# Kernel optimization log

Measured on AMD Instinct MI355X. Metric: run time of the kernel, lower is better.

Reference implementation:

```python
import jax, jax.numpy as jnp
import numpy as np

B, S, H = 32, 4096, 512

def setup_inputs() -> dict:
    key = jax.random.key(0)
    k1, k2, k3 = jax.random.split(key, 3)
    h_t = jax.random.normal(k1, (B, H), dtype=jnp.float32)
    context = jax.random.normal(k2, (B, S, H), dtype=jnp.float32)
    W = jax.random.normal(k3, (H, H), dtype=jnp.float32) * (1.0 / np.sqrt(H))
    pos = 7  # current cyclic-buffer write index (self.it % seq_len)
    return {"h_t": h_t, "context": context, "W": W, "pos": pos}

def reference(h_t, context, W, pos):
    # Luong 'general' attention: score[b,s] = h_t[b] . (W @ context[b,s])
    scores = jnp.einsum('bh,hk,bsk->bs', h_t, W, context)  # [B,S]
    attn = jax.nn.softmax(scores, axis=-1)                  # softmax over buffer slots
    # weighted sum over the context buffer -> [B,H]
    cntx = jnp.einsum('bs,bsh->bh', attn, context)
    # cyclic buffer write: add_vector(h_t) at slot pos (detached in original)
    new_buffer = context.at[:, pos % context.shape[1], :].set(h_t)
    return cntx, new_buffer
```

## Files before the change

### kernel.cpp

```cpp
#include <hip/hip_runtime.h>
#include <math.h>

constexpr int B = 32, S = 4096, H = 512;
constexpr int BDIM = 256;
constexpr int MAX_SPLIT = 128;
constexpr float LOG2E = 1.44269504088896340736f;
constexpr float DEFER_THR = 11.5415603f;

typedef float f4 __attribute__((ext_vector_type(4)));

__global__ __launch_bounds__(BDIM) void u_kernel(const float* __restrict__ h_t,
                                                 const float* __restrict__ W,
                                                 float* __restrict__ u) {
    const int b = blockIdx.y;
    const int k = blockIdx.x * BDIM + threadIdx.x;
    __shared__ float hs[H];
    for (int i = threadIdx.x; i < H; i += BDIM) hs[i] = h_t[b * H + i];
    __syncthreads();
    float a0 = 0.f, a1 = 0.f, a2 = 0.f, a3 = 0.f;
#pragma unroll 8
    for (int h = 0; h < H; h += 4) {
        a0 = fmaf(hs[h],     W[(size_t)(h)     * H + k], a0);
        a1 = fmaf(hs[h + 1], W[(size_t)(h + 1) * H + k], a1);
        a2 = fmaf(hs[h + 2], W[(size_t)(h + 2) * H + k], a2);
        a3 = fmaf(hs[h + 3], W[(size_t)(h + 3) * H + k], a3);
    }
    u[b * H + k] = ((a0 + a1) + (a2 + a3)) * LOG2E;
}

__global__ __launch_bounds__(BDIM) void flash_kernel(const float* __restrict__ ctx,
                                                     const float* __restrict__ u,
                                                     float* __restrict__ newbuf,
                                                     float* __restrict__ pacc,
                                                     float* __restrict__ pml,
                                                     int nsplit) {
    const int b     = blockIdx.y;
    const int split = blockIdx.x;
    const int w     = threadIdx.x >> 6;
    const int lane  = threadIdx.x & 63;
    const int g     = lane >> 5;
    const int j     = lane & 31;
    const int rpb   = S / nsplit;
    const int rpw   = rpb / 4;
    const int s0    = split * rpb + w * rpw;

    const f4* ub = (const f4*)(u + (size_t)b * H);
    f4 uf[4];
#pragma unroll
    for (int k = 0; k < 4; ++k) uf[k] = ub[j + 32 * k];

    float m = -INFINITY, l = 0.f;
    f4 acc[4] = {{0,0,0,0},{0,0,0,0},{0,0,0,0},{0,0,0,0}};

#pragma unroll 2
    for (int r = 0; r < rpw; r += 2) {
        const size_t row = (size_t)b * S + s0 + r + g;
        const f4* crow = (const f4*)(ctx + row * H);
        f4 c[4];
#pragma unroll
        for (int k = 0; k < 4; ++k) c[k] = crow[j + 32 * k];

        f4* orow = (f4*)(newbuf + row * H);
#pragma unroll
        for (int k = 0; k < 4; ++k)
            __builtin_nontemporal_store(c[k], orow + j + 32 * k);

        float d = c[0].x * uf[0].x;
        d = fmaf(c[0].y, uf[0].y, d); d = fmaf(c[0].z, uf[0].z, d);
        d = fmaf(c[0].w, uf[0].w, d);
#pragma unroll
        for (int k = 1; k < 4; ++k) {
            d = fmaf(c[k].x, uf[k].x, d); d = fmaf(c[k].y, uf[k].y, d);
            d = fmaf(c[k].z, uf[k].z, d); d = fmaf(c[k].w, uf[k].w, d);
        }
#pragma unroll
        for (int off = 16; off >= 1; off >>= 1) d += __shfl_xor(d, off);

        if (d > m + DEFER_THR) {
            const float sc = exp2f(m - d);
#pragma unroll
            for (int k = 0; k < 4; ++k) acc[k] *= sc;
            l *= sc; m = d;
        }
        const float p = exp2f(d - m);
#pragma unroll
        for (int k = 0; k < 4; ++k) acc[k] += p * c[k];
        l += p;
    }

    const float mo = __shfl_xor(m, 32);
    const float lo = __shfl_xor(l, 32);
    const float M  = fmaxf(m, mo);
    const float es = exp2f(m - M), eo = exp2f(mo - M);
    const float lw = es * l + eo * lo;
    f4 am[4];
#pragma unroll
    for (int k = 0; k < 4; ++k) {
        f4 other;
        other.x = __shfl_xor(acc[k].x, 32);
        other.y = __shfl_xor(acc[k].y, 32);
        other.z = __shfl_xor(acc[k].z, 32);
        other.w = __shfl_xor(acc[k].w, 32);
        am[k] = es * acc[k] + eo * other;
    }

    __shared__ float lacc[4][H];
    __shared__ float lml[4][2];
    if (g == 0) {
        f4* dst = (f4*)&lacc[w][0];
#pragma unroll
        for (int k = 0; k < 4; ++k) dst[j + 32 * k] = am[k];
        if (j == 0) { lml[w][0] = M; lml[w][1] = lw; }
    }
    __syncthreads();

    const float m0 = lml[0][0], m1 = lml[1][0], m2 = lml[2][0], m3 = lml[3][0];
    const float Mb = fmaxf(fmaxf(m0, m1), fmaxf(m2, m3));
    const float e0 = exp2f(m0 - Mb), e1 = exp2f(m1 - Mb);
    const float e2 = exp2f(m2 - Mb), e3 = exp2f(m3 - Mb);

    const int t    = threadIdx.x;
    const int pidx = b * nsplit + split;
    const float ca = e0 * lacc[0][t]       + e1 * lacc[1][t]
                   + e2 * lacc[2][t]       + e3 * lacc[3][t];
    const float cb = e0 * lacc[0][256 + t] + e1 * lacc[1][256 + t]
                   + e2 * lacc[2][256 + t] + e3 * lacc[3][256 + t];
    pacc[(size_t)pidx * H + t]       = ca;
    pacc[(size_t)pidx * H + 256 + t] = cb;
    if (t == 0) {
        const float L = e0 * lml[0][1] + e1 * lml[1][1]
                      + e2 * lml[2][1] + e3 * lml[3][1];
        pml[2 * pidx] = Mb; pml[2 * pidx + 1] = L;
    }
}

__global__ __launch_bounds__(BDIM) void combine_kernel(const float* __restrict__ pacc,
                                                       const float* __restrict__ pml,
                                                       const float* __restrict__ h_t,
                                                       const int* __restrict__ posp,
                                                       float* __restrict__ newbuf,
                                                       float* __restrict__ cntx,
                                                       int nsplit) {
    const int b    = blockIdx.x;
    const int half = blockIdx.y;
    const int t    = threadIdx.x;
    const int col  = half * 256 + t;

    int pos = posp[0] % S; if (pos < 0) pos += S;
    newbuf[((size_t)b * S + pos) * H + col] = h_t[b * H + col];

    __shared__ float lm[MAX_SPLIT], ll[MAX_SPLIT];
    for (int p = t; p < nsplit; p += BDIM) {
        lm[p] = pml[2 * (b * nsplit + p)];
        ll[p] = pml[2 * (b * nsplit + p) + 1];
    }
    __syncthreads();

    float M = -INFINITY;
    for (int p = 0; p < nsplit; ++p) M = fmaxf(M, lm[p]);

    float acc = 0.f, L = 0.f;
#pragma unroll 4
    for (int p = 0; p < nsplit; ++p) {
        const float e = exp2f(lm[p] - M);
        L   = fmaf(e, ll[p], L);
        acc = fmaf(e, pacc[(size_t)(b * nsplit + p) * H + col], acc);
    }
    cntx[b * H + col] = acc / L;
}

extern "C" void kernel_launch(void* const* d_in, const int* in_sizes, int n_in,
                              void* d_out, int out_size, void* d_ws, size_t ws_size,
                              hipStream_t stream) {
    const float* h_t = (const float*)d_in[0];
    const float* ctx = (const float*)d_in[1];
    const float* W   = (const float*)d_in[2];
    const int*   pos = (const int*)d_in[3];

    float* out    = (float*)d_out;
    float* cntx   = out;
    float* newbuf = out + (size_t)B * H;

    char*  ws = (char*)d_ws;
    float* u  = (float*)ws;
    const size_t u_bytes = (size_t)B * H * sizeof(float);

    int nsplit = MAX_SPLIT;
    while (nsplit > 1) {
        const size_t need = u_bytes
                          + (size_t)B * nsplit * H * sizeof(float)
                          + (size_t)B * nsplit * 2 * sizeof(float);
        if (need <= ws_size) break;
        nsplit >>= 1;
    }
    float* pacc = (float*)(ws + u_bytes);
    float* pml  = pacc + (size_t)B * nsplit * H;

    u_kernel<<<dim3(H / BDIM, B), BDIM, 0, stream>>>(h_t, W, u);
    flash_kernel<<<dim3(nsplit, B), BDIM, 0, stream>>>(ctx, u, newbuf,
                                                       pacc, pml, nsplit);
    combine_kernel<<<dim3(B, 2), BDIM, 0, stream>>>(pacc, pml, h_t, pos,
                                                    newbuf, cntx, nsplit);
}
```

Measured before the change: 122.2 us.

## Halve flash block size and interleave two independent online-softmax streams per wave

The flash kernel now runs 128 threads (2 waves) per block instead of 256. Each wave covers twice as many rows, split into two independent halves (A and B) with separate running max, sum and accumulator. Interleaving the two streams raises memory-level parallelism and ILP per wave, and the loop is fully unrolled. The cost is higher register pressure and fewer waves resident per block, with the per-block reduction rewritten for two waves and a vectorized partial write.

```diff
diff --git a/kernel.cpp b/kernel.cpp
--- a/kernel.cpp
+++ b/kernel.cpp
@@ -2,20 +2,21 @@
 #include <math.h>
 
 constexpr int B = 32, S = 4096, H = 512;
-constexpr int BDIM = 256;
+constexpr int UDIM = 256;
+constexpr int FDIM = 128;
 constexpr int MAX_SPLIT = 128;
 constexpr float LOG2E = 1.44269504088896340736f;
 constexpr float DEFER_THR = 11.5415603f;
 
 typedef float f4 __attribute__((ext_vector_type(4)));
 
-__global__ __launch_bounds__(BDIM) void u_kernel(const float* __restrict__ h_t,
+__global__ __launch_bounds__(UDIM) void u_kernel(const float* __restrict__ h_t,
                                                  const float* __restrict__ W,
                                                  float* __restrict__ u) {
     const int b = blockIdx.y;
-    const int k = blockIdx.x * BDIM + threadIdx.x;
+    const int k = blockIdx.x * UDIM + threadIdx.x;
     __shared__ float hs[H];
-    for (int i = threadIdx.x; i < H; i += BDIM) hs[i] = h_t[b * H + i];
+    for (int i = threadIdx.x; i < H; i += UDIM) hs[i] = h_t[b * H + i];
     __syncthreads();
     float a0 = 0.f, a1 = 0.f, a2 = 0.f, a3 = 0.f;
 #pragma unroll 8
@@ -28,7 +29,7 @@
     u[b * H + k] = ((a0 + a1) + (a2 + a3)) * LOG2E;
 }
 
-__global__ __launch_bounds__(BDIM) void flash_kernel(const float* __restrict__ ctx,
+__global__ __launch_bounds__(FDIM) void flash_kernel(const float* __restrict__ ctx,
                                                      const float* __restrict__ u,
                                                      float* __restrict__ newbuf,
                                                      float* __restrict__ pacc,
@@ -41,7 +42,8 @@
     const int g     = lane >> 5;
     const int j     = lane & 31;
     const int rpb   = S / nsplit;
-    const int rpw   = rpb / 4;
+    const int rpw   = rpb / 2;
+    const int hrw   = rpw / 2;
     const int s0    = split * rpb + w * rpw;
 
     const f4* ub = (const f4*)(u + (size_t)b * H);
@@ -49,98 +51,130 @@
 #pragma unroll
     for (int k = 0; k < 4; ++k) uf[k] = ub[j + 32 * k];
 
-    float m = -INFINITY, l = 0.f;
-    f4 acc[4] = {{0,0,0,0},{0,0,0,0},{0,0,0,0},{0,0,0,0}};
-
-#pragma unroll 2
-    for (int r = 0; r < rpw; r += 2) {
-        const size_t row = (size_t)b * S + s0 + r + g;
-        const f4* crow = (const f4*)(ctx + row * H);
-        f4 c[4];
-#pragma unroll
-        for (int k = 0; k < 4; ++k) c[k] = crow[j + 32 * k];
-
-        f4* orow = (f4*)(newbuf + row * H);
-#pragma unroll
-        for (int k = 0; k < 4; ++k)
-            __builtin_nontemporal_store(c[k], orow + j + 32 * k);
-
-        float d = c[0].x * uf[0].x;
-        d = fmaf(c[0].y, uf[0].y, d); d = fmaf(c[0].z, uf[0].z, d);
-        d = fmaf(c[0].w, uf[0].w, d);
+    const size_t baseA = (size_t)b * S + s0;
+    const size_t baseB = baseA + hrw;
+
+    float mA = -INFINITY, lA = 0.f;
+    float mB = -INFINITY, lB = 0.f;
+    f4 accA[4] = {{0,0,0,0},{0,0,0,0},{0,0,0,0},{0,0,0,0}};
+    f4 accB[4] = {{0,0,0,0},{0,0,0,0},{0,0,0,0},{0,0,0,0}};
+
+#pragma unroll
+    for (int r = 0; r < hrw; r += 2) {
+        const size_t rowA = baseA + r + g;
+        const size_t rowB = baseB + r + g;
+        const f4* cra = (const f4*)(ctx + rowA * H);
+        const f4* crb = (const f4*)(ctx + rowB * H);
+        f4 cA[4], cB[4];
+#pragma unroll
+        for (int k = 0; k < 4; ++k) cA[k] = cra[j + 32 * k];
+#pragma unroll
+        for (int k = 0; k < 4; ++k) cB[k] = crb[j + 32 * k];
+
+        f4* oa = (f4*)(newbuf + rowA * H);
+        f4* ob = (f4*)(newbuf + rowB * H);
+#pragma unroll
+        for (int k = 0; k < 4; ++k) {
+            __builtin_nontemporal_store(cA[k], oa + j + 32 * k);
+            __builtin_nontemporal_store(cB[k], ob + j + 32 * k);
+        }
+
+        float dA = cA[0].x * uf[0].x, dB = cB[0].x * uf[0].x;
+        dA = fmaf(cA[0].y, uf[0].y, dA); dB = fmaf(cB[0].y, uf[0].y, dB);
+        dA = fmaf(cA[0].z, uf[0].z, dA); dB = fmaf(cB[0].z, uf[0].z, dB);
+        dA = fmaf(cA[0].w, uf[0].w, dA); dB = fmaf(cB[0].w, uf[0].w, dB);
 #pragma unroll
         for (int k = 1; k < 4; ++k) {
-            d = fmaf(c[k].x, uf[k].x, d); d = fmaf(c[k].y, uf[k].y, d);
-            d = fmaf(c[k].z, uf[k].z, d); d = fmaf(c[k].w, uf[k].w, d);
-        }
-#pragma unroll
-        for (int off = 16; off >= 1; off >>= 1) d += __shfl_xor(d, off);
-
-        if (d > m + DEFER_THR) {
-            const float sc = exp2f(m - d);
-#pragma unroll
-            for (int k = 0; k < 4; ++k) acc[k] *= sc;
-            l *= sc; m = d;
-        }
-        const float p = exp2f(d - m);
-#pragma unroll
-        for (int k = 0; k < 4; ++k) acc[k] += p * c[k];
-        l += p;
-    }
-
-    const float mo = __shfl_xor(m, 32);
-    const float lo = __shfl_xor(l, 32);
-    const float M  = fmaxf(m, mo);
-    const float es = exp2f(m - M), eo = exp2f(mo - M);
-    const float lw = es * l + eo * lo;
+            dA = fmaf(cA[k].x, uf[k].x, dA); dB = fmaf(cB[k].x, uf[k].x, dB);
+            dA = fmaf(cA[k].y, uf[k].y, dA); dB = fmaf(cB[k].y, uf[k].y, dB);
+            dA = fmaf(cA[k].z, uf[k].z, dA); dB = fmaf(cB[k].z, uf[k].z, dB);
+            dA = fmaf(cA[k].w, uf[k].w, dA); dB = fmaf(cB[k].w, uf[k].w, dB);
+        }
+#pragma unroll
+        for (int off = 16; off >= 1; off >>= 1) {
+            dA += __shfl_xor(dA, off);
+            dB += __shfl_xor(dB, off);
+        }
+
+        if (dA > mA + DEFER_THR) {
+            const float sc = exp2f(mA - dA);
+#pragma unroll
+            for (int k = 0; k < 4; ++k) accA[k] *= sc;
+            lA *= sc; mA = dA;
+        }
+        if (dB > mB + DEFER_THR) {
+            const float sc = exp2f(mB - dB);
+#pragma unroll
+            for (int k = 0; k < 4; ++k) accB[k] *= sc;
+            lB *= sc; mB = dB;
+        }
+        const float pA = exp2f(dA - mA);
+        const float pB = exp2f(dB - mB);
+#pragma unroll
+        for (int k = 0; k < 4; ++k) {
+            accA[k] += pA * cA[k];
+            accB[k] += pB * cB[k];
+        }
+        lA += pA; lB += pB;
+    }
+
+    const float moA = __shfl_xor(mA, 32), loA = __shfl_xor(lA, 32);
+    const float moB = __shfl_xor(mB, 32), loB = __shfl_xor(lB, 32);
+    const float MA = fmaxf(mA, moA), MB = fmaxf(mB, moB);
+    const float esA = exp2f(mA - MA), eoA = exp2f(moA - MA);
+    const float esB = exp2f(mB - MB), eoB = exp2f(moB - MB);
+    const float lwA = esA * lA + eoA * loA;
+    const float lwB = esB * lB + eoB * loB;
+#pragma unroll
+    for (int k = 0; k < 4; ++k) {
+        f4 oA, oB;
+        oA.x = __shfl_xor(accA[k].x, 32); oB.x = __shfl_xor(accB[k].x, 32);
+        oA.y = __shfl_xor(accA[k].y, 32); oB.y = __shfl_xor(accB[k].y, 32);
+        oA.z = __shfl_xor(accA[k].z, 32); oB.z = __shfl_xor(accB[k].z, 32);
+        oA.w = __shfl_xor(accA[k].w, 32); oB.w = __shfl_xor(accB[k].w, 32);
+        accA[k] = esA * accA[k] + eoA * oA;
+        accB[k] = esB * accB[k] + eoB * oB;
+    }
+    const float Mw = fmaxf(MA, MB);
+    const float eA = exp2f(MA - Mw), eB = exp2f(MB - Mw);
+    const float lw = eA * lwA + eB * lwB;
     f4 am[4];
 #pragma unroll
-    for (int k = 0; k < 4; ++k) {
-        f4 other;
-        other.x = __shfl_xor(acc[k].x, 32);
-        other.y = __shfl_xor(acc[k].y, 32);
-        other.z = __shfl_xor(acc[k].z, 32);
-        other.w = __shfl_xor(acc[k].w, 32);
-        am[k] = es * acc[k] + eo * other;
-    }
-
-    __shared__ float lacc[4][H];
-    __shared__ float lml[4][2];
+    for (int k = 0; k < 4; ++k) am[k] = eA * accA[k] + eB * accB[k];
+
+    __shared__ float lacc[2][H];
+    __shared__ float lml[2][2];
     if (g == 0) {
         f4* dst = (f4*)&lacc[w][0];
 #pragma unroll
         for (int k = 0; k < 4; ++k) dst[j + 32 * k] = am[k];
-        if (j == 0) { lml[w][0] = M; lml[w][1] = lw; }
+        if (j == 0) { lml[w][0] = Mw; lml[w][1] = lw; }
     }
     __syncthreads();
 
-    const float m0 = lml[0][0], m1 = lml[1][0], m2 = lml[2][0], m3 = lml[3][0];
-    const float Mb = fmaxf(fmaxf(m0, m1), fmaxf(m2, m3));
+    const float m0 = lml[0][0], m1 = lml[1][0];
+    const float Mb = fmaxf(m0, m1);
     const float e0 = exp2f(m0 - Mb), e1 = exp2f(m1 - Mb);
-    const float e2 = exp2f(m2 - Mb), e3 = exp2f(m3 - Mb);
 
     const int t    = threadIdx.x;
     const int pidx = b * nsplit + split;
-    const float ca = e0 * lacc[0][t]       + e1 * lacc[1][t]
-                   + e2 * lacc[2][t]       + e3 * lacc[3][t];
-    const float cb = e0 * lacc[0][256 + t] + e1 * lacc[1][256 + t]
-                   + e2 * lacc[2][256 + t] + e3 * lacc[3][256 + t];
-    pacc[(size_t)pidx * H + t]       = ca;
-    pacc[(size_t)pidx * H + 256 + t] = cb;
+    f4* pa = (f4*)(pacc + (size_t)pidx * H);
+    const f4* l0 = (const f4*)&lacc[0][0];
+    const f4* l1 = (const f4*)&lacc[1][0];
+    pa[t] = e0 * l0[t] + e1 * l1[t];
     if (t == 0) {
-        const float L = e0 * lml[0][1] + e1 * lml[1][1]
-                      + e2 * lml[2][1] + e3 * lml[3][1];
+        const float L = e0 * lml[0][1] + e1 * lml[1][1];
         pml[2 * pidx] = Mb; pml[2 * pidx + 1] = L;
     }
 }
 
-__global__ __launch_bounds__(BDIM) void combine_kernel(const float* __restrict__ pacc,
-                                                       const float* __restrict__ pml,
-                                                       const float* __restrict__ h_t,
-                                                       const int* __restrict__ posp,
-                                                       float* __restrict__ newbuf,
-                                                       float* __restrict__ cntx,
-                                                       int nsplit) {
+__global__ __launch_bounds__(256) void combine_kernel(const float* __restrict__ pacc,
+                                                      const float* __restrict__ pml,
+                                                      const float* __restrict__ h_t,
+                                                      const int* __restrict__ posp,
+                                                      float* __restrict__ newbuf,
+                                                      float* __restrict__ cntx,
+                                                      int nsplit) {
     const int b    = blockIdx.x;
     const int half = blockIdx.y;
     const int t    = threadIdx.x;
@@ -150,7 +184,7 @@
     newbuf[((size_t)b * S + pos) * H + col] = h_t[b * H + col];
 
     __shared__ float lm[MAX_SPLIT], ll[MAX_SPLIT];
-    for (int p = t; p < nsplit; p += BDIM) {
+    for (int p = t; p < nsplit; p += 256) {
         lm[p] = pml[2 * (b * nsplit + p)];
         ll[p] = pml[2 * (b * nsplit + p) + 1];
     }
@@ -196,9 +230,9 @@
     float* pacc = (float*)(ws + u_bytes);
     float* pml  = pacc + (size_t)B * nsplit * H;
 
-    u_kernel<<<dim3(H / BDIM, B), BDIM, 0, stream>>>(h_t, W, u);
-    flash_kernel<<<dim3(nsplit, B), BDIM, 0, stream>>>(ctx, u, newbuf,
+    u_kernel<<<dim3(H / UDIM, B), UDIM, 0, stream>>>(h_t, W, u);
+    flash_kernel<<<dim3(nsplit, B), FDIM, 0, stream>>>(ctx, u, newbuf,
                                                        pacc, pml, nsplit);
-    combine_kernel<<<dim3(B, 2), BDIM, 0, stream>>>(pacc, pml, h_t, pos,
-                                                    newbuf, cntx, nsplit);
-}
+    combine_kernel<<<dim3(B, 2), 256, 0, stream>>>(pacc, pml, h_t, pos,
+                                                   newbuf, cntx, nsplit);
+}
```

Result: slower. 125.3 us (+2.6%).
